# Performance work log

Hardware: AMD Instinct MI355X
Metric: run time of the kernel (lower is better)

Reference implementation:

```python
import jax, jax.numpy as jnp
import numpy as np

NB, MS, T, IN, H, OUT, DOCS, ENT = 512, 8, 64, 360, 230, 53, 32, 8


def setup_inputs() -> dict:
    key = jax.random.key(0)
    ks = jax.random.split(key, 16)
    s = 0.05
    inp = {
        "bag": jax.random.normal(ks[0], (NB, MS, T, IN), jnp.float32),
        "W_ih_f": jax.random.normal(ks[1], (3 * H, IN), jnp.float32) * s,
        "W_hh_f": jax.random.normal(ks[2], (3 * H, H), jnp.float32) * s,
        "b_ih_f": jnp.zeros((3 * H,), jnp.float32),
        "b_hh_f": jnp.zeros((3 * H,), jnp.float32),
        "W_ih_r": jax.random.normal(ks[3], (3 * H, IN), jnp.float32) * s,
        "W_hh_r": jax.random.normal(ks[4], (3 * H, H), jnp.float32) * s,
        "b_ih_r": jnp.zeros((3 * H,), jnp.float32),
        "b_hh_r": jnp.zeros((3 * H,), jnp.float32),
        "W_word": jax.random.normal(ks[5], (2 * H, 2 * H), jnp.float32) * s,
        "b_word": jnp.zeros((2 * H,), jnp.float32),
        "proj_word": jax.random.normal(ks[6], (2 * H,), jnp.float32) * s,
        "W_sent": jax.random.normal(ks[7], (2 * H, 2 * H), jnp.float32) * s,
        "b_sent": jnp.zeros((2 * H,), jnp.float32),
        "proj_sent": jax.random.normal(ks[8], (2 * H,), jnp.float32) * s,
        "fc_W": jax.random.normal(ks[9], (OUT, 2 * H), jnp.float32) * s,
        "fc_b": jnp.zeros((OUT,), jnp.float32),
    }
    # unique (doc, ent_a, ent_b) triples with a != b, as the Python bag loop produces
    rng = np.random.RandomState(0)
    grid = np.stack(np.meshgrid(np.arange(DOCS), np.arange(ENT), np.arange(ENT), indexing="ij"), -1).reshape(-1, 3)
    grid = grid[grid[:, 1] != grid[:, 2]]
    inp["pairs"] = jnp.asarray(grid[rng.permutation(len(grid))[:NB]], jnp.int32)
    return inp


def _gru_dir(xg, W_hh, b_hh, reverse):
    # xg: [T, B, 3H] precomputed input-gate projections; torch gate order r,z,n
    def step(h, xt):
        hg = h @ W_hh.T + b_hh  # [B, 3H]
        r = jax.nn.sigmoid(xt[:, :H] + hg[:, :H])
        z = jax.nn.sigmoid(xt[:, H:2 * H] + hg[:, H:2 * H])
        n = jnp.tanh(xt[:, 2 * H:] + r * hg[:, 2 * H:])
        h2 = (1.0 - z) * n + z * h
        return h2, h2
    h0 = jnp.zeros((xg.shape[1], H), xg.dtype)
    _, hs = jax.lax.scan(step, h0, xg, reverse=reverse)
    return hs  # [T, B, H], time-aligned


def reference(bag, W_ih_f, W_hh_f, b_ih_f, b_hh_f, W_ih_r, W_hh_r, b_ih_r, b_hh_r,
              W_word, b_word, proj_word, W_sent, b_sent, proj_sent, fc_W, fc_b, pairs):
    B = NB * MS
    # every sentence of every bag runs through the same GRU -> batch them all
    x = bag.reshape(B, T, IN).transpose(1, 0, 2)  # [T, B, IN]
    hf = _gru_dir(x @ W_ih_f.T + b_ih_f, W_hh_f, b_hh_f, reverse=False)
    hr = _gru_dir(x @ W_ih_r.T + b_ih_r, W_hh_r, b_hh_r, reverse=True)
    out = jnp.concatenate([hf, hr], axis=-1)  # [T, B, 2H]
    # word-level tanh attention over time
    u = jnp.tanh(out @ W_word + b_word)
    alpha = jax.nn.softmax(u @ proj_word, axis=0)  # [T, B]
    word_vec = jnp.einsum("tb,tbh->bh", alpha, out)  # [B, 2H]
    word_vec = word_vec.reshape(NB, MS, 2 * H).transpose(1, 0, 2)  # [MS, NB, 2H]
    # sentence-level tanh attention over sentences in each bag
    u2 = jnp.tanh(word_vec @ W_sent + b_sent)
    beta = jax.nn.softmax(u2 @ proj_sent, axis=0)  # [MS, NB]
    sent_vec = jnp.einsum("sb,sbh->bh", beta, word_vec)  # [NB, 2H]
    bag_out = sent_vec @ fc_W.T + fc_b  # [NB, OUT]
    # scatter bag outputs into the dense (doc, ent_a, ent_b) result tensor
    bags_res = jnp.zeros((DOCS, ENT, ENT, OUT), bag_out.dtype)
    bags_res = bags_res.at[pairs[:, 0], pairs[:, 1], pairs[:, 2]].set(bag_out)
    return bags_res
```

## Files before the change

### kernel.cpp

```cpp
#include <hip/hip_runtime.h>
#include <math.h>

typedef __bf16 bf16;
typedef __bf16 bf16x8 __attribute__((ext_vector_type(8)));
typedef float f32x4 __attribute__((ext_vector_type(4)));
typedef float f4 __attribute__((ext_vector_type(4)));

constexpr int kNB = 512, kMS = 8, kT = 64, kH = 230, kIN = 360, kOUT = 53;
constexpr int kB  = kNB * kMS;
constexpr long kBT = (long)kB * kT;
constexpr int kNP  = 768;
constexpr int kKIH = 384;
constexpr int kKHH = 256;
constexpr int k2H  = 460;
constexpr int kLD  = 464;
constexpr int kKW  = 480;
constexpr int kXS  = 772;
constexpr int kHB  = 268;

__device__ inline float fast_sigmoid(float x) {
    return __builtin_amdgcn_rcpf(1.f + __builtin_amdgcn_exp2f(x * -1.442695040888963f));
}
__device__ inline float fast_tanh(float x) {
    return 1.f - 2.f * __builtin_amdgcn_rcpf(1.f + __builtin_amdgcn_exp2f(x * 2.885390081777927f));
}

constexpr long SZ_XG    = 2L * kB * kT * kNP * 2;
constexpr long SZ_OUT   = kBT * kLD * 2;
constexpr long SZ_WIHP  = 2L * kNP * kKIH * 2;
constexpr long SZ_WHHP  = 2L * kNP * kKHH * 2;
constexpr long SZ_WWT   = 512L * kKW * 2;
constexpr long SZ_WST   = 512L * kKW * 2;
constexpr long SZ_BIHP  = 2L * kNP * 4;
constexpr long SZ_BHHP  = 2L * kNP * 4;
constexpr long SZ_VEC   = 2048L * 4;
constexpr long SZ_SCORE = kBT * 4;
constexpr long SZ_WVF   = (long)kB * kLD * 4;
constexpr long SZ_WVB   = (long)kB * kLD * 2;
constexpr long SZ_S2    = (long)kB * 4;

static inline long align256(long x) { return (x + 255) & ~255L; }

constexpr int R0 = 2 * kNP * kKIH;
constexpr int R1 = 2 * kNP * kKHH;
constexpr int R2 = 512 * kKW;
constexpr int R3 = 512 * kKW;
constexpr int R4 = 2 * kNP;
constexpr int R5 = 2 * kNP;
constexpr int R6 = 4 * 512;
constexpr long PREP_TOTAL = (long)R0 + R1 + R2 + R3 + R4 + R5 + R6;

__device__ inline bool unpack_n(int n, int& src) {
    int cb = n / 48, w = n % 48, g = w / 16, cc = w & 15;
    int c = cb * 16 + cc;
    src = g * kH + c;
    return c < kH;
}

__launch_bounds__(256)
__global__ void prep_pack(const float* __restrict__ Wihf, const float* __restrict__ Wihr,
                          const float* __restrict__ Whhf, const float* __restrict__ Whhr,
                          const float* __restrict__ bihf, const float* __restrict__ bihr,
                          const float* __restrict__ bhhf, const float* __restrict__ bhhr,
                          const float* __restrict__ Ww,  const float* __restrict__ bw,
                          const float* __restrict__ pw,
                          const float* __restrict__ Wsn, const float* __restrict__ bs,
                          const float* __restrict__ ps,
                          bf16* __restrict__ WihP, bf16* __restrict__ WhhP,
                          bf16* __restrict__ WwT,  bf16* __restrict__ WsT,
                          float* __restrict__ bihP, float* __restrict__ bhhP,
                          float* __restrict__ vecP)
{
    for (long id = (long)blockIdx.x * 256 + threadIdx.x; id < PREP_TOTAL;
         id += (long)gridDim.x * 256) {
        long i = id;
        if (i < R0) {
            int d = (int)(i / (kNP * kKIH)); int r = (int)(i % (kNP * kKIH));
            int n = r / kKIH, k = r % kKIH;
            int src; bool v = unpack_n(n, src) && (k < kIN);
            WihP[i] = v ? (bf16)(d ? Wihr : Wihf)[(long)src * kIN + k] : (bf16)0.f;
            continue;
        }
        i -= R0;
        if (i < R1) {
            int d = (int)(i / (kNP * kKHH)); int r = (int)(i % (kNP * kKHH));
            int n = r / kKHH, k = r % kKHH;
            int src; bool v = unpack_n(n, src) && (k < kH);
            WhhP[i] = v ? (bf16)(d ? Whhr : Whhf)[(long)src * kH + k] : (bf16)0.f;
            continue;
        }
        i -= R1;
        if (i < R2) {
            int n = (int)(i / kKW), k = (int)(i % kKW);
            WwT[i] = (n < k2H && k < k2H) ? (bf16)Ww[(long)k * k2H + n] : (bf16)0.f;
            continue;
        }
        i -= R2;
        if (i < R3) {
            int n = (int)(i / kKW), k = (int)(i % kKW);
            WsT[i] = (n < k2H && k < k2H) ? (bf16)Wsn[(long)k * k2H + n] : (bf16)0.f;
            continue;
        }
        i -= R3;
        if (i < R4) {
            int d = (int)(i / kNP), n = (int)(i % kNP);
            int src; bool v = unpack_n(n, src);
            bihP[i] = v ? (d ? bihr : bihf)[src] : 0.f;
            continue;
        }
        i -= R4;
        if (i < R5) {
            int d = (int)(i / kNP), n = (int)(i % kNP);
            int src; bool v = unpack_n(n, src);
            bhhP[i] = v ? (d ? bhhr : bhhf)[src] : 0.f;
            continue;
        }
        i -= R5;
        {
            int which = (int)(i / 512), n = (int)(i % 512);
            const float* s = (which == 0) ? bw : (which == 1) ? pw : (which == 2) ? bs : ps;
            vecP[i] = (n < k2H) ? s[n] : 0.f;
        }
    }
}

template<int MODE, typename AT>
__launch_bounds__(256)
__global__ void gemm_k(const AT* __restrict__ A, int lda, int K, int ksteps,
                       const bf16* __restrict__ Bp, long bStride,
                       bf16* __restrict__ C, int ldc, long cStride,
                       const float* __restrict__ bias, int biasStride,
                       const float* __restrict__ proj,
                       float* __restrict__ score,
                       int nblks, int zc)
{
    __shared__ bf16 As[128][40];
    __shared__ bf16 Bs[128][40];
    const int tid = threadIdx.x;
    const int grp = 8 * nblks * zc;
    const int mg = blockIdx.x / grp, sub = blockIdx.x % grp;
    const int mi = sub & 7, rest = sub >> 3;
    const int nblk = rest % nblks, z = rest / nblks;
    const int mblk = mg * 8 + mi;

    const bf16* Bz = Bp + (long)z * bStride;
    const int rowA0 = mblk * 128, rowB0 = nblk * 128;
    const int lane = tid & 63, wave = tid >> 6;
    const int wm = wave >> 1, wn = wave & 1;
    const int quad = lane >> 4, l16 = lane & 15;
    const int ldb = ksteps * 32;

    const int sr0 = tid >> 2, sk0 = (tid & 3) * 8;
    const int sr1 = sr0 + 64;

    f32x4 acc[4][4] = {};

    for (int ks = 0; ks < ksteps; ++ks) {
        const int kk = ks * 32 + sk0;
        const int v = K - kk;
        {
            const AT* pa0 = A + (long)(rowA0 + sr0) * lda + kk;
            const AT* pa1 = A + (long)(rowA0 + sr1) * lda + kk;
            bf16x8 v0, v1;
            if (v >= 8) {
                if constexpr (sizeof(AT) == 2) {
                    v0 = *(const bf16x8*)pa0;
                    v1 = *(const bf16x8*)pa1;
                } else {
                    const f4* p0 = (const f4*)pa0; f4 a0 = p0[0], b0 = p0[1];
                    const f4* p1 = (const f4*)pa1; f4 a1 = p1[0], b1 = p1[1];
                    v0[0]=(bf16)a0[0]; v0[1]=(bf16)a0[1]; v0[2]=(bf16)a0[2]; v0[3]=(bf16)a0[3];
                    v0[4]=(bf16)b0[0]; v0[5]=(bf16)b0[1]; v0[6]=(bf16)b0[2]; v0[7]=(bf16)b0[3];
                    v1[0]=(bf16)a1[0]; v1[1]=(bf16)a1[1]; v1[2]=(bf16)a1[2]; v1[3]=(bf16)a1[3];
                    v1[4]=(bf16)b1[0]; v1[5]=(bf16)b1[1]; v1[6]=(bf16)b1[2]; v1[7]=(bf16)b1[3];
                }
            } else {
                for (int j = 0; j < 8; ++j) {
                    ((bf16*)&v0)[j] = (j < v) ? (bf16)(float)pa0[j] : (bf16)0.f;
                    ((bf16*)&v1)[j] = (j < v) ? (bf16)(float)pa1[j] : (bf16)0.f;
                }
            }
            *(bf16x8*)&As[sr0][sk0] = v0;
            *(bf16x8*)&As[sr1][sk0] = v1;
            *(bf16x8*)&Bs[sr0][sk0] = *(const bf16x8*)(Bz + (long)(rowB0 + sr0) * ldb + kk);
            *(bf16x8*)&Bs[sr1][sk0] = *(const bf16x8*)(Bz + (long)(rowB0 + sr1) * ldb + kk);
        }
        __syncthreads();
        bf16x8 af[4], bfr[4];
#pragma unroll
        for (int mt = 0; mt < 4; ++mt) af[mt] = *(const bf16x8*)&As[wm * 64 + mt * 16 + l16][quad * 8];
#pragma unroll
        for (int nt = 0; nt < 4; ++nt) bfr[nt] = *(const bf16x8*)&Bs[wn * 64 + nt * 16 + l16][quad * 8];
#pragma unroll
        for (int mt = 0; mt < 4; ++mt)
#pragma unroll
            for (int nt = 0; nt < 4; ++nt)
                acc[mt][nt] = __builtin_amdgcn_mfma_f32_16x16x32_bf16(af[mt], bfr[nt], acc[mt][nt], 0, 0, 0);
        __syncthreads();
    }

    if constexpr (MODE == 0 || MODE == 2) {
        bf16* Cz = C + (long)z * cStride;
        const float* bz = bias + (long)z * biasStride;
#pragma unroll
        for (int mt = 0; mt < 4; ++mt)
#pragma unroll
            for (int nt = 0; nt < 4; ++nt) {
                const int col = rowB0 + wn * 64 + nt * 16 + l16;
                const float bv = bz[col];
#pragma unroll
                for (int r = 0; r < 4; ++r) {
                    const int row = rowA0 + wm * 64 + mt * 16 + quad * 4 + r;
                    const int rowp = (MODE == 2) ? ((row & 63) * kB + (row >> 6)) : row;
                    Cz[(long)rowp * ldc + col] = (bf16)(acc[mt][nt][r] + bv);
                }
            }
    } else {
#pragma unroll
        for (int mt = 0; mt < 4; ++mt)
#pragma unroll
            for (int r = 0; r < 4; ++r) {
                float s = 0.f;
#pragma unroll
                for (int nt = 0; nt < 4; ++nt) {
                    const int col = rowB0 + wn * 64 + nt * 16 + l16;
                    s += fast_tanh(acc[mt][nt][r] + bias[col]) * proj[col];
                }
                for (int m = 1; m < 16; m <<= 1) s += __shfl_xor(s, m, 64);
                if (l16 == 0) {
                    const int row = rowA0 + wm * 64 + mt * 16 + quad * 4 + r;
                    atomicAdd(&score[row], s);
                }
            }
    }
}

__launch_bounds__(512)
__global__ void gru_rec(const bf16* __restrict__ xg,
                        const bf16* __restrict__ Whh,
                        const float* __restrict__ bhh,
                        bf16* __restrict__ outbuf)
{
    __shared__ bf16 hbf[32][kHB];
    __shared__ bf16 xs[32][kXS];
    const int tid = threadIdx.x;
    const int d = blockIdx.y;
    const int row0 = blockIdx.x * 32;
    const int lane = tid & 63, wave = tid >> 6;
    const int quad = lane >> 4, l16 = lane & 15;
    const int cb0 = wave * 2;

    for (int i = tid; i < 32 * kHB; i += 512) (&hbf[0][0])[i] = (bf16)0.f;

    const bf16* xgd = xg + (long)d * ((long)kT * kB * kNP);
    const bf16* Wd  = Whh + (long)d * ((long)kNP * kKHH);
    const float* bd = bhh + (long)d * kNP;

    float hreg[2][2][4] = {};
    float bdr[2], bdz[2], bdn[2];
#pragma unroll
    for (int cbl = 0; cbl < 2; ++cbl) {
        const int cb = cb0 + cbl;
        bdr[cbl] = bd[cb * 48 + l16];
        bdz[cbl] = bd[cb * 48 + 16 + l16];
        bdn[cbl] = bd[cb * 48 + 32 + l16];
    }

    const int xr_row = tid >> 4, xr_col = (tid & 15) * 48;

    bf16x8 pf[6];
    {
        const int t0 = d ? kT - 1 : 0;
        const bf16* src = xgd + ((long)t0 * kB + row0) * kNP + (long)tid * 48;
#pragma unroll
        for (int j = 0; j < 6; ++j) pf[j] = *(const bf16x8*)(src + j * 8);
    }
    __syncthreads();

    for (int it = 0; it < kT; ++it) {
        const int t = d ? (kT - 1 - it) : it;
#pragma unroll
        for (int j = 0; j < 6; ++j) *(bf16x8*)&xs[xr_row][xr_col + j * 8] = pf[j];

        f32x4 acc[2][2][3] = {};
#pragma unroll
        for (int ks = 0; ks < 8; ++ks) {
            bf16x8 af0 = *(const bf16x8*)&hbf[l16][ks * 32 + quad * 8];
            bf16x8 af1 = *(const bf16x8*)&hbf[16 + l16][ks * 32 + quad * 8];
#pragma unroll
            for (int cbl = 0; cbl < 2; ++cbl)
#pragma unroll
                for (int g = 0; g < 3; ++g) {
                    const int n = (cb0 + cbl) * 48 + g * 16 + l16;
                    bf16x8 bfr = *(const bf16x8*)(Wd + (long)n * kKHH + ks * 32 + quad * 8);
                    acc[0][cbl][g] = __builtin_amdgcn_mfma_f32_16x16x32_bf16(af0, bfr, acc[0][cbl][g], 0, 0, 0);
                    acc[1][cbl][g] = __builtin_amdgcn_mfma_f32_16x16x32_bf16(af1, bfr, acc[1][cbl][g], 0, 0, 0);
                }
        }
        if (it + 1 < kT) {
            const int tn = d ? (kT - 2 - it) : (it + 1);
            const bf16* src = xgd + ((long)tn * kB + row0) * kNP + (long)tid * 48;
#pragma unroll
            for (int j = 0; j < 6; ++j) pf[j] = *(const bf16x8*)(src + j * 8);
        }
        __syncthreads();

#pragma unroll
        for (int cbl = 0; cbl < 2; ++cbl) {
            const int cb = cb0 + cbl;
            const int c = cb * 16 + l16;
            if (c < kH) {
#pragma unroll
                for (int mt = 0; mt < 2; ++mt)
#pragma unroll
                    for (int r = 0; r < 4; ++r) {
                        const int rl = mt * 16 + quad * 4 + r;
                        const float xr = (float)xs[rl][cb * 48 + l16];
                        const float xz = (float)xs[rl][cb * 48 + 16 + l16];
                        const float xn = (float)xs[rl][cb * 48 + 32 + l16];
                        const float rgate = fast_sigmoid(xr + acc[mt][cbl][0][r] + bdr[cbl]);
                        const float zgate = fast_sigmoid(xz + acc[mt][cbl][1][r] + bdz[cbl]);
                        const float ngate = fast_tanh(xn + rgate * (acc[mt][cbl][2][r] + bdn[cbl]));
                        const float h2 = (1.f - zgate) * ngate + zgate * hreg[mt][cbl][r];
                        hreg[mt][cbl][r] = h2;
                        hbf[rl][c] = (bf16)h2;
                        outbuf[((long)(row0 + rl) * kT + t) * kLD + d * kH + c] = (bf16)h2;
                    }
            }
        }
        __syncthreads();
    }
}

__launch_bounds__(256)
__global__ void word_attn(const float* __restrict__ score, const bf16* __restrict__ outbuf,
                          float* __restrict__ wvf, bf16* __restrict__ wvb)
{
    const int b = blockIdx.x, tid = threadIdx.x;
    __shared__ float alpha[kT];
    if (tid < 64) {
        float v = score[b * kT + tid];
        float m = v;
        for (int off = 32; off; off >>= 1) m = fmaxf(m, __shfl_xor(m, off, 64));
        float e = __builtin_amdgcn_exp2f((v - m) * 1.442695040888963f);
        float s = e;
        for (int off = 32; off; off >>= 1) s += __shfl_xor(s, off, 64);
        alpha[tid] = e / s;
    }
    __syncthreads();
    const bf16* base = outbuf + (long)b * kT * kLD;
    float a0 = 0.f, a1 = 0.f;
    const int c0 = tid, c1 = tid + 256;
#pragma unroll 4
    for (int t = 0; t < kT; ++t) {
        const float al = alpha[t];
        a0 += al * (float)base[t * kLD + c0];
        if (c1 < k2H) a1 += al * (float)base[t * kLD + c1];
    }
    wvf[(long)b * kLD + c0] = a0;
    wvb[(long)b * kLD + c0] = (bf16)a0;
    if (c1 < k2H) {
        wvf[(long)b * kLD + c1] = a1;
        wvb[(long)b * kLD + c1] = (bf16)a1;
    }
}

__launch_bounds__(256)
__global__ void final_sent(const float* __restrict__ score2, const float* __restrict__ wvf,
                           const float* __restrict__ fcW, const float* __restrict__ fcb,
                           const int* __restrict__ pairs, float* __restrict__ outp)
{
    const int nb = blockIdx.x, tid = threadIdx.x;
    __shared__ float beta[kMS];
    __shared__ float sv[k2H];
    if (tid == 0) {
        float m = -1e30f;
        for (int s = 0; s < kMS; ++s) m = fmaxf(m, score2[nb * kMS + s]);
        float e[kMS], sum = 0.f;
        for (int s = 0; s < kMS; ++s) { e[s] = expf(score2[nb * kMS + s] - m); sum += e[s]; }
        for (int s = 0; s < kMS; ++s) beta[s] = e[s] / sum;
    }
    __syncthreads();
    for (int c = tid; c < k2H; c += 256) {
        float a = 0.f;
#pragma unroll
        for (int s = 0; s < kMS; ++s) a += beta[s] * wvf[(long)(nb * kMS + s) * kLD + c];
        sv[c] = a;
    }
    __syncthreads();
    const int lane = tid & 63, wave = tid >> 6;
    const long base = ((long)pairs[nb * 3] * 64 + pairs[nb * 3 + 1] * 8 + pairs[nb * 3 + 2]) * kOUT;
    for (int o = wave; o < kOUT; o += 4) {
        float p = 0.f;
        for (int c = lane; c < k2H; c += 64) p += sv[c] * fcW[(long)o * k2H + c];
        for (int off = 32; off; off >>= 1) p += __shfl_xor(p, off, 64);
        if (lane == 0) outp[base + o] = p + fcb[o];
    }
}

extern "C" void kernel_launch(void* const* d_in, const int* in_sizes, int n_in,
                              void* d_out, int out_size, void* d_ws, size_t ws_size,
                              hipStream_t stream)
{
    const float* bag  = (const float*)d_in[0];
    const float* Wihf = (const float*)d_in[1];
    const float* Whhf = (const float*)d_in[2];
    const float* bihf = (const float*)d_in[3];
    const float* bhhf = (const float*)d_in[4];
    const float* Wihr = (const float*)d_in[5];
    const float* Whhr = (const float*)d_in[6];
    const float* bihr = (const float*)d_in[7];
    const float* bhhr = (const float*)d_in[8];
    const float* Ww   = (const float*)d_in[9];
    const float* bw   = (const float*)d_in[10];
    const float* pw   = (const float*)d_in[11];
    const float* Wsn  = (const float*)d_in[12];
    const float* bs   = (const float*)d_in[13];
    const float* ps   = (const float*)d_in[14];
    const float* fcW  = (const float*)d_in[15];
    const float* fcb  = (const float*)d_in[16];
    const int* pairs  = (const int*)d_in[17];

    char* ws = (char*)d_ws;
    long off = 0;
    auto alloc = [&](long sz) { void* p = ws + off; off += align256(sz); return p; };
    bf16* xg    = (bf16*)alloc(SZ_XG);
    bf16* outb  = (bf16*)alloc(SZ_OUT);
    bf16* WihP  = (bf16*)alloc(SZ_WIHP);
    bf16* WhhP  = (bf16*)alloc(SZ_WHHP);
    bf16* WwT   = (bf16*)alloc(SZ_WWT);
    bf16* WsT   = (bf16*)alloc(SZ_WST);
    float* bihP = (float*)alloc(SZ_BIHP);
    float* bhhP = (float*)alloc(SZ_BHHP);
    float* vecP = (float*)alloc(SZ_VEC);
    float* score= (float*)alloc(SZ_SCORE);
    float* wvf  = (float*)alloc(SZ_WVF);
    bf16* wvb   = (bf16*)alloc(SZ_WVB);
    float* s2   = (float*)alloc(SZ_S2);
    if ((size_t)off > ws_size) return;

    hipMemsetAsync(d_out, 0, (size_t)out_size * 4, stream);
    hipMemsetAsync(score, 0, SZ_SCORE, stream);
    hipMemsetAsync(s2, 0, SZ_S2, stream);

    prep_pack<<<5781, 256, 0, stream>>>(Wihf, Wihr, Whhf, Whhr, bihf, bihr, bhhf, bhhr,
                                        Ww, bw, pw, Wsn, bs, ps,
                                        WihP, WhhP, WwT, WsT, bihP, bhhP, vecP);

    gemm_k<2, float><<<2048 * 6 * 2, 256, 0, stream>>>(bag, kIN, kIN, 12,
                                                       WihP, (long)kNP * kKIH,
                                                       xg, kNP, (long)kT * kB * kNP,
                                                       bihP, kNP, nullptr, nullptr, 6, 2);

    gru_rec<<<dim3(128, 2), 512, 0, stream>>>(xg, WhhP, bhhP, outb);

    gemm_k<1, bf16><<<2048 * 4, 256, 0, stream>>>(outb, kLD, k2H, 15,
                                                  WwT, 0, nullptr, 0, 0,
                                                  vecP, 0, vecP + 512, score, 4, 1);

    word_attn<<<kB, 256, 0, stream>>>(score, outb, wvf, wvb);

    gemm_k<1, bf16><<<32 * 4, 256, 0, stream>>>(wvb, kLD, k2H, 15,
                                                WsT, 0, nullptr, 0, 0,
                                                vecP + 1024, 0, vecP + 1536, s2, 4, 1);

    final_sent<<<kNB, 256, 0, stream>>>(s2, wvf, fcW, fcb, pairs, (float*)d_out);
}
```

Before: 2.282 ms.

## Pre-convert bag to bf16 and use direct global-to-LDS loads in GEMM

Adds a conversion kernel that turns the fp32 bag input into a zero-padded bf16 buffer, reusing the GRU output buffer as scratch. This removes the fp32-to-bf16 conversion and the K-edge masking from the input-projection GEMM. The GEMM is also rewritten to stage A and B tiles into LDS with 16-byte global_load_lds instructions instead of going through registers. The LDS tiles lose their padding, which risks bank conflicts on the fragment reads. With masking gone, the attention GEMMs now read the padded columns past K and rely on the packed weights being zero there; the extra conversion pass also adds memory traffic.

```diff
diff --git a/kernel.cpp b/kernel.cpp
--- a/kernel.cpp
+++ b/kernel.cpp
@@ -23,6 +23,11 @@
 }
 __device__ inline float fast_tanh(float x) {
     return 1.f - 2.f * __builtin_amdgcn_rcpf(1.f + __builtin_amdgcn_exp2f(x * 2.885390081777927f));
+}
+
+__device__ inline void async16(const bf16* g, void* l) {
+    __builtin_amdgcn_global_load_lds((const __attribute__((address_space(1))) void*)g,
+                                     (__attribute__((address_space(3))) void*)l, 16, 0, 0);
 }
 
 constexpr long SZ_XG    = 2L * kB * kT * kNP * 2;
@@ -41,6 +46,24 @@
 
 static inline long align256(long x) { return (x + 255) & ~255L; }
 
+__launch_bounds__(256)
+__global__ void convert_bag(const float* __restrict__ bag, bf16* __restrict__ bagb)
+{
+    const long g = (long)blockIdx.x * 256 + threadIdx.x;
+    if (g >= kBT * 48) return;
+    const long row = g / 48; const int cb = (int)(g % 48);
+    bf16x8 v;
+    if (cb < 45) {
+        const f4* p = (const f4*)(bag + row * kIN + cb * 8);
+        f4 a = p[0], b = p[1];
+        v[0]=(bf16)a[0]; v[1]=(bf16)a[1]; v[2]=(bf16)a[2]; v[3]=(bf16)a[3];
+        v[4]=(bf16)b[0]; v[5]=(bf16)b[1]; v[6]=(bf16)b[2]; v[7]=(bf16)b[3];
+    } else {
+        v = bf16x8{};
+    }
+    *(bf16x8*)(bagb + row * kKIH + cb * 8) = v;
+}
+
 constexpr int R0 = 2 * kNP * kKIH;
 constexpr int R1 = 2 * kNP * kKHH;
 constexpr int R2 = 512 * kKW;
@@ -124,9 +147,9 @@
     }
 }
 
-template<int MODE, typename AT>
+template<int MODE>
 __launch_bounds__(256)
-__global__ void gemm_k(const AT* __restrict__ A, int lda, int K, int ksteps,
+__global__ void gemm_k(const bf16* __restrict__ A, int lda, int ksteps,
                        const bf16* __restrict__ Bp, long bStride,
                        bf16* __restrict__ C, int ldc, long cStride,
                        const float* __restrict__ bias, int biasStride,
@@ -134,8 +157,8 @@
                        float* __restrict__ score,
                        int nblks, int zc)
 {
-    __shared__ bf16 As[128][40];
-    __shared__ bf16 Bs[128][40];
+    __shared__ bf16 As[128][32];
+    __shared__ bf16 Bs[128][32];
     const int tid = threadIdx.x;
     const int grp = 8 * nblks * zc;
     const int mg = blockIdx.x / grp, sub = blockIdx.x % grp;
@@ -150,41 +173,24 @@
     const int quad = lane >> 4, l16 = lane & 15;
     const int ldb = ksteps * 32;
 
-    const int sr0 = tid >> 2, sk0 = (tid & 3) * 8;
-    const int sr1 = sr0 + 64;
+    const int sr = lane >> 2, scb = (lane & 3) * 8;
+    const bf16* gA0 = A + (long)(rowA0 + wave * 16 + sr) * lda + scb;
+    const bf16* gA1 = gA0 + (long)64 * lda;
+    const bf16* gB0 = Bz + (long)(rowB0 + wave * 16 + sr) * ldb + scb;
+    const bf16* gB1 = gB0 + (long)64 * ldb;
+    void* lA0 = &As[wave * 16][0];
+    void* lA1 = &As[64 + wave * 16][0];
+    void* lB0 = &Bs[wave * 16][0];
+    void* lB1 = &Bs[64 + wave * 16][0];
 
     f32x4 acc[4][4] = {};
 
     for (int ks = 0; ks < ksteps; ++ks) {
-        const int kk = ks * 32 + sk0;
-        const int v = K - kk;
-        {
-            const AT* pa0 = A + (long)(rowA0 + sr0) * lda + kk;
-            const AT* pa1 = A + (long)(rowA0 + sr1) * lda + kk;
-            bf16x8 v0, v1;
-            if (v >= 8) {
-                if constexpr (sizeof(AT) == 2) {
-                    v0 = *(const bf16x8*)pa0;
-                    v1 = *(const bf16x8*)pa1;
-                } else {
-                    const f4* p0 = (const f4*)pa0; f4 a0 = p0[0], b0 = p0[1];
-                    const f4* p1 = (const f4*)pa1; f4 a1 = p1[0], b1 = p1[1];
-                    v0[0]=(bf16)a0[0]; v0[1]=(bf16)a0[1]; v0[2]=(bf16)a0[2]; v0[3]=(bf16)a0[3];
-                    v0[4]=(bf16)b0[0]; v0[5]=(bf16)b0[1]; v0[6]=(bf16)b0[2]; v0[7]=(bf16)b0[3];
-                    v1[0]=(bf16)a1[0]; v1[1]=(bf16)a1[1]; v1[2]=(bf16)a1[2]; v1[3]=(bf16)a1[3];
-                    v1[4]=(bf16)b1[0]; v1[5]=(bf16)b1[1]; v1[6]=(bf16)b1[2]; v1[7]=(bf16)b1[3];
-                }
-            } else {
-                for (int j = 0; j < 8; ++j) {
-                    ((bf16*)&v0)[j] = (j < v) ? (bf16)(float)pa0[j] : (bf16)0.f;
-                    ((bf16*)&v1)[j] = (j < v) ? (bf16)(float)pa1[j] : (bf16)0.f;
-                }
-            }
-            *(bf16x8*)&As[sr0][sk0] = v0;
-            *(bf16x8*)&As[sr1][sk0] = v1;
-            *(bf16x8*)&Bs[sr0][sk0] = *(const bf16x8*)(Bz + (long)(rowB0 + sr0) * ldb + kk);
-            *(bf16x8*)&Bs[sr1][sk0] = *(const bf16x8*)(Bz + (long)(rowB0 + sr1) * ldb + kk);
-        }
+        const int kk = ks * 32;
+        async16(gA0 + kk, lA0);
+        async16(gA1 + kk, lA1);
+        async16(gB0 + kk, lB0);
+        async16(gB1 + kk, lB1);
         __syncthreads();
         bf16x8 af[4], bfr[4];
 #pragma unroll
@@ -426,6 +432,7 @@
     auto alloc = [&](long sz) { void* p = ws + off; off += align256(sz); return p; };
     bf16* xg    = (bf16*)alloc(SZ_XG);
     bf16* outb  = (bf16*)alloc(SZ_OUT);
+    bf16* bagb  = outb;
     bf16* WihP  = (bf16*)alloc(SZ_WIHP);
     bf16* WhhP  = (bf16*)alloc(SZ_WHHP);
     bf16* WwT   = (bf16*)alloc(SZ_WWT);
@@ -443,26 +450,28 @@
     hipMemsetAsync(score, 0, SZ_SCORE, stream);
     hipMemsetAsync(s2, 0, SZ_S2, stream);
 
+    convert_bag<<<(int)((kBT * 48 + 255) / 256), 256, 0, stream>>>(bag, bagb);
+
     prep_pack<<<5781, 256, 0, stream>>>(Wihf, Wihr, Whhf, Whhr, bihf, bihr, bhhf, bhhr,
                                         Ww, bw, pw, Wsn, bs, ps,
                                         WihP, WhhP, WwT, WsT, bihP, bhhP, vecP);
 
-    gemm_k<2, float><<<2048 * 6 * 2, 256, 0, stream>>>(bag, kIN, kIN, 12,
-                                                       WihP, (long)kNP * kKIH,
-                                                       xg, kNP, (long)kT * kB * kNP,
-                                                       bihP, kNP, nullptr, nullptr, 6, 2);
+    gemm_k<2><<<2048 * 6 * 2, 256, 0, stream>>>(bagb, kKIH, 12,
+                                                WihP, (long)kNP * kKIH,
+                                                xg, kNP, (long)kT * kB * kNP,
+                                                bihP, kNP, nullptr, nullptr, 6, 2);
 
     gru_rec<<<dim3(128, 2), 512, 0, stream>>>(xg, WhhP, bhhP, outb);
 
-    gemm_k<1, bf16><<<2048 * 4, 256, 0, stream>>>(outb, kLD, k2H, 15,
-                                                  WwT, 0, nullptr, 0, 0,
-                                                  vecP, 0, vecP + 512, score, 4, 1);
+    gemm_k<1><<<2048 * 4, 256, 0, stream>>>(outb, kLD, 15,
+                                            WwT, 0, nullptr, 0, 0,
+                                            vecP, 0, vecP + 512, score, 4, 1);
 
     word_attn<<<kB, 256, 0, stream>>>(score, outb, wvf, wvb);
 
-    gemm_k<1, bf16><<<32 * 4, 256, 0, stream>>>(wvb, kLD, k2H, 15,
-                                                WsT, 0, nullptr, 0, 0,
-                                                vecP + 1024, 0, vecP + 1536, s2, 4, 1);
+    gemm_k<1><<<32 * 4, 256, 0, stream>>>(wvb, kLD, 15,
+                                          WsT, 0, nullptr, 0, 0,
+                                          vecP + 1024, 0, vecP + 1536, s2, 4, 1);
 
     final_sent<<<kNB, 256, 0, stream>>>(s2, wvf, fcW, fcb, pairs, (float*)d_out);
 }
```

Result: faster. 2.154 ms (-5.6%).
